# Kernel tuning notes

Hardware: AMD Instinct MI355X
Metric: run time of the kernel (lower is better)

The kernel has to match this reference:

```python
import jax, jax.numpy as jnp
import numpy as np

DN = ('NCDHW', 'OIDHW', 'NCDHW')


def conv3d(x, w, b, stride=2, pad=1):
    # w: [Cout, Cin, k, k, k] (PyTorch Conv3d layout == OIDHW)
    y = jax.lax.conv_general_dilated(x, w, (stride,) * 3, [(pad, pad)] * 3,
                                     dimension_numbers=DN)
    return y + b[None, :, None, None, None]


def convT3d(x, w, b, stride=2, pad=1):
    # w: [Cin, Cout, k, k, k] (PyTorch ConvTranspose3d layout).
    # ConvTranspose(k,s,p) == conv(lhs_dilated by s, flipped kernel, pad = k-1-p)
    k = w.shape[2]
    wf = jnp.transpose(jnp.flip(w, (2, 3, 4)), (1, 0, 2, 3, 4))  # -> OIDHW
    p = k - 1 - pad
    y = jax.lax.conv_general_dilated(x, wf, (1, 1, 1), [(p, p)] * 3,
                                     lhs_dilation=(stride,) * 3,
                                     dimension_numbers=DN)
    return y + b[None, :, None, None, None]


def setup_inputs() -> dict:
    key = jax.random.key(0)
    ks = jax.random.split(key, 14)
    s = 0.05
    inp = {
        'x': jax.random.normal(ks[0], (4, 1, 128, 128, 128), jnp.float32),
        # encoder conv weights (OIDHW) + biases
        'w1': jax.random.normal(ks[1], (16, 1, 4, 4, 4), jnp.float32) * s,
        'b1': jnp.zeros((16,), jnp.float32),
        'w2': jax.random.normal(ks[2], (32, 16, 4, 4, 4), jnp.float32) * s,
        'b2': jnp.zeros((32,), jnp.float32),
        'w3': jax.random.normal(ks[3], (64, 32, 4, 4, 4), jnp.float32) * s,
        'b3': jnp.zeros((64,), jnp.float32),
        # VQ codebook [num_embeddings=512, latent_dim=64]
        'codebook': jax.random.normal(ks[4], (512, 64), jnp.float32),
        # decoder conv-transpose weights (PyTorch layout: [Cin, Cout, k,k,k]) + biases
        'dw1': jax.random.normal(ks[5], (64, 32, 4, 4, 4), jnp.float32) * s,
        'db1': jnp.zeros((32,), jnp.float32),
        'dw2': jax.random.normal(ks[6], (32, 16, 4, 4, 4), jnp.float32) * s,
        'db2': jnp.zeros((16,), jnp.float32),
        'dw3': jax.random.normal(ks[7], (16, 1, 4, 4, 4), jnp.float32) * s,
        'db3': jnp.zeros((1,), jnp.float32),
    }
    return inp


def reference(x, w1, b1, w2, b2, w3, b3, codebook, dw1, db1, dw2, db2, dw3, db3):
    # ---- encoder ----
    h = jax.nn.relu(conv3d(x, w1, b1))
    h = jax.nn.relu(conv3d(h, w2, b2))
    z_e = conv3d(h, w3, b3)                      # [B, C=64, D, H, W]
    B, C, D, H, W = z_e.shape

    # ---- vector quantization (cdist + argmin + gather) ----
    zf = jnp.transpose(z_e.reshape(B, C, -1), (0, 2, 1))   # [B, N, C]
    # squared euclidean distances (argmin identical to cdist argmin)
    d2 = (jnp.sum(zf * zf, axis=-1, keepdims=True)
          + jnp.sum(codebook * codebook, axis=-1)[None, None, :]
          - 2.0 * jnp.einsum('bnc,kc->bnk', zf, codebook))  # [B, N, K]
    encoding_indices = jnp.argmin(d2, axis=-1)              # [B, N]
    q = codebook[encoding_indices]                          # [B, N, C]
    quantized = jnp.transpose(q, (0, 2, 1)).reshape(B, C, D, H, W)
    # straight-through estimator
    quantized = z_e + jax.lax.stop_gradient(quantized - z_e)

    # ---- decoder ----
    h = jax.nn.relu(convT3d(quantized, dw1, db1))
    h = jax.nn.relu(convT3d(h, dw2, db2))
    x_hat = jax.nn.sigmoid(convT3d(h, dw3, db3))
    return (x_hat, quantized, z_e)
```

## Files before the change

### kernel.cpp

```cpp
#include <hip/hip_runtime.h>
#include <math.h>


__device__ __forceinline__ float4 ld4(const float* p) {
  float4 q; __builtin_memcpy(&q, p, 16); return q;
}
struct F3 { float x, y, z; };
__device__ __forceinline__ F3 ld3(const float* p) {
  F3 q; __builtin_memcpy(&q, p, 12); return q;
}

#define WAVES_HINT __attribute__((amdgpu_waves_per_eu(2, 4)))

template<int CIN, int COUT>
__global__ __launch_bounds__(256) void k_repackT(const float* __restrict__ w,
                                                 float* __restrict__ dst) {
  const int idx = blockIdx.x * 256 + threadIdx.x;
  if (idx >= CIN * 8 * COUT * 8) return;
  const int a  = idx & 7;
  const int co = (idx >> 3) % COUT;
  const int p  = ((idx >> 3) / COUT) & 7;
  const int ci2 = idx / (8 * COUT * 8);
  const int az = a >> 2, ay = (a >> 1) & 1, ax = a & 1;
  const int pz = p >> 2, py = (p >> 1) & 1, px = p & 1;
  const int kz = 3 - pz - 2 * az, ky = 3 - py - 2 * ay, kx = 3 - px - 2 * ax;
  dst[(((size_t)(ci2 * 8 + p) * COUT + co) * 16) + az * 8 + (ay * 2 + ax)] =
      w[((size_t)ci2 * COUT + co) * 64 + (kz * 16 + ky * 4 + kx)];
}

template<int S, int D, int NCH>
__global__ __launch_bounds__(256) void k_zhalo(float* __restrict__ buf) {
  const int vol = S * S * S;
  const long long idx = (long long)blockIdx.x * 256 + threadIdx.x;
  if (idx >= (long long)NCH * vol) return;
  const int r = (int)(idx % vol);
  const int z = r / (S * S), y = (r / S) % S, x = r % S;
  if (z < 1 || z > D || y < 1 || y > D || x < 1 || x > D) buf[idx] = 0.0f;
}

template<int CIN, int COUT, int DIN, int DOUT, int OCG, int TZ, bool RELU,
         bool INP, int SIN, bool OUTP, int SOUT, int NG>
__global__ __launch_bounds__(256) WAVES_HINT
void k_conv(const float* __restrict__ xin, const float* __restrict__ wg,
            const float* __restrict__ bias, float* __restrict__ out) {
  constexpr int NBX = DOUT / 8, NBY = DOUT / 8, NBZ = DOUT / (4 * TZ);
  constexpr size_t VIN  = INP  ? (size_t)SIN * SIN * SIN : (size_t)DIN * DIN * DIN;
  constexpr size_t VOUT = OUTP ? (size_t)SOUT * SOUT * SOUT : (size_t)DOUT * DOUT * DOUT;
  const int tid = threadIdx.x;
  const int tx = tid & 7, ty = (tid >> 3) & 7, tz = tid >> 6;
  int bb = blockIdx.x;
  const int g  = bb % NG;  bb /= NG;
  const int gx = bb % NBX; bb /= NBX;
  const int gy = bb % NBY; bb /= NBY;
  const int gz = bb % NBZ; bb /= NBZ;
  const int b = bb;
  const int oc0 = g * OCG;
  const int ow = gx * 8 + tx, oh = gy * 8 + ty, od0 = gz * (4 * TZ) + tz;

  float acc[TZ][OCG];
#pragma unroll
  for (int j = 0; j < TZ; ++j)
#pragma unroll
    for (int c = 0; c < OCG; ++c) acc[j][c] = 0.0f;

#pragma unroll 1
  for (int ci = 0; ci < CIN; ++ci) {
    const float* xb = xin + (size_t)(b * CIN + ci) * VIN;
#pragma unroll 1
    for (int t16 = 0; t16 < 16; ++t16) {
      float4 q[TZ];
      if (INP) {
        const int zp = od0 * 2 + (t16 >> 2);
        const int yp = oh * 2 + (t16 & 3);
        const float* r0 = xb + ((size_t)zp * SIN + yp) * SIN + ow * 2;
#pragma unroll
        for (int j = 0; j < TZ; ++j) q[j] = ld4(r0 + (size_t)j * 8 * SIN * SIN);
      } else {
        const int y  = oh * 2 - 1 + (t16 & 3);
        const int x0 = ow * 2 - 1;
        const bool vy = (unsigned)y < (unsigned)DIN;
#pragma unroll
        for (int j = 0; j < TZ; ++j) {
          const int z = od0 * 2 - 1 + (t16 >> 2) + j * 8;
          const bool vz = vy && ((unsigned)z < (unsigned)DIN);
          const float* xr = xb + ((size_t)z * DIN + y) * DIN + x0;
          q[j].x = (vz && (unsigned)(x0 + 0) < (unsigned)DIN) ? xr[0] : 0.0f;
          q[j].y = (vz && (unsigned)(x0 + 1) < (unsigned)DIN) ? xr[1] : 0.0f;
          q[j].z = (vz && (unsigned)(x0 + 2) < (unsigned)DIN) ? xr[2] : 0.0f;
          q[j].w = (vz && (unsigned)(x0 + 3) < (unsigned)DIN) ? xr[3] : 0.0f;
        }
      }
#pragma unroll
      for (int c = 0; c < OCG; ++c) {
        const float4 w4 = ld4(wg + ((size_t)(oc0 + c) * CIN + ci) * 64 + t16 * 4);
#pragma unroll
        for (int j = 0; j < TZ; ++j) {
          acc[j][c] = fmaf(q[j].x, w4.x, acc[j][c]);
          acc[j][c] = fmaf(q[j].y, w4.y, acc[j][c]);
          acc[j][c] = fmaf(q[j].z, w4.z, acc[j][c]);
          acc[j][c] = fmaf(q[j].w, w4.w, acc[j][c]);
        }
      }
    }
  }

#pragma unroll
  for (int c = 0; c < OCG; ++c) {
    const float bv = bias[oc0 + c];
#pragma unroll
    for (int j = 0; j < TZ; ++j) {
      float v = acc[j][c] + bv;
      if (RELU) v = fmaxf(v, 0.0f);
      const int od = od0 + j * 4;
      if (OUTP)
        out[(size_t)(b * COUT + oc0 + c) * VOUT
            + ((size_t)(od + 1) * SOUT + (oh + 1)) * SOUT + (ow + 1)] = v;
      else
        out[(size_t)(b * COUT + oc0 + c) * VOUT
            + ((size_t)od * DOUT + oh) * DOUT + ow] = v;
    }
  }
}

template<int CIN, int COUT, int DIN, int OCG, int TZ, int EPI, int SIN,
         bool OUTP, int SOUT, int NG>
__global__ __launch_bounds__(256) WAVES_HINT
void k_convt(const float* __restrict__ xin, const float* __restrict__ wp,
             const float* __restrict__ bias, float* __restrict__ out) {
  constexpr int DOUT = 2 * DIN, NBX = DIN / 8, NBY = DIN / 8,
                NBZ = DIN / (4 * TZ);
  constexpr size_t VIN  = (size_t)SIN * SIN * SIN;
  constexpr size_t VOUT = OUTP ? (size_t)SOUT * SOUT * SOUT
                               : (size_t)DOUT * DOUT * DOUT;
  const int tid = threadIdx.x;
  const int tx = tid & 7, ty = (tid >> 3) & 7, tz = tid >> 6;
  int bb = blockIdx.x;
  const int g  = bb % NG;  bb /= NG;
  const int gx = bb % NBX; bb /= NBX;
  const int gy = bb % NBY; bb /= NBY;
  const int gz = bb % NBZ; bb /= NBZ;
  const int b = bb;
  const int oc0 = g * OCG;
  const int mx = gx * 8 + tx, my = gy * 8 + ty;
  const int mz0 = gz * (4 * TZ) + tz * TZ;

  float acc[TZ][8][OCG];
#pragma unroll
  for (int j = 0; j < TZ; ++j)
#pragma unroll
    for (int p = 0; p < 8; ++p)
#pragma unroll
      for (int c = 0; c < OCG; ++c) acc[j][p][c] = 0.0f;

#pragma unroll 1
  for (int ci = 0; ci < CIN; ++ci) {
    const float* xb = xin + (size_t)(b * CIN + ci) * VIN
                          + ((size_t)mz0 * SIN + my) * SIN + mx;
    float xn[TZ + 2][3][3];
#pragma unroll
    for (int dz = 0; dz < TZ + 2; ++dz)
#pragma unroll
      for (int dy = 0; dy < 3; ++dy) {
        const F3 t = ld3(xb + ((size_t)dz * SIN + dy) * SIN);
        xn[dz][dy][0] = t.x; xn[dz][dy][1] = t.y; xn[dz][dy][2] = t.z;
      }
    __builtin_amdgcn_sched_barrier(0);

    const float* wci = wp + (size_t)ci * 8 * COUT * 16;
#pragma unroll
    for (int p = 0; p < 8; ++p) {
      const int pz = p >> 2, py = (p >> 1) & 1, px = p & 1;
#pragma unroll
      for (int c = 0; c < OCG; ++c) {
        const float* wb = wci + ((size_t)p * COUT + (oc0 + c)) * 16;
        const float4 wA = ld4(wb);
        const float4 wB = ld4(wb + 8);
#pragma unroll
        for (int j = 0; j < TZ; ++j)
          acc[j][p][c] = fmaf(xn[j + pz][py    ][px    ], wA.x, acc[j][p][c]);
#pragma unroll
        for (int j = 0; j < TZ; ++j)
          acc[j][p][c] = fmaf(xn[j + pz][py    ][px + 1], wA.y, acc[j][p][c]);
#pragma unroll
        for (int j = 0; j < TZ; ++j)
          acc[j][p][c] = fmaf(xn[j + pz][py + 1][px    ], wA.z, acc[j][p][c]);
#pragma unroll
        for (int j = 0; j < TZ; ++j)
          acc[j][p][c] = fmaf(xn[j + pz][py + 1][px + 1], wA.w, acc[j][p][c]);
#pragma unroll
        for (int j = 0; j < TZ; ++j)
          acc[j][p][c] = fmaf(xn[j + pz + 1][py    ][px    ], wB.x, acc[j][p][c]);
#pragma unroll
        for (int j = 0; j < TZ; ++j)
          acc[j][p][c] = fmaf(xn[j + pz + 1][py    ][px + 1], wB.y, acc[j][p][c]);
#pragma unroll
        for (int j = 0; j < TZ; ++j)
          acc[j][p][c] = fmaf(xn[j + pz + 1][py + 1][px    ], wB.z, acc[j][p][c]);
#pragma unroll
        for (int j = 0; j < TZ; ++j)
          acc[j][p][c] = fmaf(xn[j + pz + 1][py + 1][px + 1], wB.w, acc[j][p][c]);
      }
    }
  }

#pragma unroll
  for (int c = 0; c < OCG; ++c) {
    const float bv = bias[oc0 + c];
#pragma unroll
    for (int j = 0; j < TZ; ++j) {
      const int mz = mz0 + j;
#pragma unroll
      for (int p = 0; p < 8; ++p) {
        const int pz = p >> 2, py = (p >> 1) & 1, px = p & 1;
        float v = acc[j][p][c] + bv;
        if (EPI == 1) v = fmaxf(v, 0.0f);
        if (EPI == 2) v = 1.0f / (1.0f + expf(-v));
        if (OUTP)
          out[(size_t)(b * COUT + oc0 + c) * VOUT
              + ((size_t)(2 * mz + pz + 1) * SOUT + (2 * my + py + 1)) * SOUT
              + (2 * mx + px + 1)] = v;
        else
          out[(size_t)(b * COUT + oc0 + c) * VOUT
              + ((size_t)(2 * mz + pz) * DOUT + (2 * my + py)) * DOUT
              + (2 * mx + px)] = v;
      }
    }
  }
}

__global__ __launch_bounds__(256) void k_vq(const float* __restrict__ ze,
                                            const float* __restrict__ cb,
                                            float* __restrict__ quant,
                                            float* __restrict__ quantp) {
  __shared__ float ct[64 * 65];
  __shared__ float zs[4][64];
  __shared__ int   bis[4];
  const int tid  = threadIdx.x;
  const int lane = tid & 63;
  const int wv   = tid >> 6;
  const int p0 = blockIdx.x * 4;
  const int b  = p0 >> 12;
  const int n0 = p0 & 4095;

  {
    const int c = tid >> 2, j = tid & 3;
    zs[j][c] = ze[((size_t)(b * 64 + c) << 12) + n0 + j];
  }

  float best = 3.4e38f;
  int bi = 0;
#pragma unroll 1
  for (int ch = 0; ch < 8; ++ch) {
    __syncthreads();
    for (int i = tid; i < 4096; i += 256) {
      const int r = i >> 6, c = i & 63;
      ct[r * 65 + c] = cb[((ch * 64 + r) << 6) + c];
    }
    __syncthreads();
    float d = 0.0f;
#pragma unroll 8
    for (int c = 0; c < 64; ++c) {
      const float t = zs[wv][c] - ct[lane * 65 + c];
      d = fmaf(t, t, d);
    }
    const int k = ch * 64 + lane;
    if (d < best) { best = d; bi = k; }
  }
#pragma unroll
  for (int off = 32; off > 0; off >>= 1) {
    const float ob = __shfl_down(best, off);
    const int   oi = __shfl_down(bi, off);
    if (ob < best || (ob == best && oi < bi)) { best = ob; bi = oi; }
  }
  if (lane == 0) bis[wv] = bi;
  __syncthreads();
  {
    const int c = tid >> 2, j = tid & 3;
    const float val = cb[(bis[j] << 6) + c];
    const int n = n0 + j;
    quant[((size_t)(b * 64 + c) << 12) + n] = val;
    const int zz = n >> 8, yy = (n >> 4) & 15, xx = n & 15;
    quantp[(size_t)(b * 64 + c) * 8000
           + ((size_t)(zz + 1) * 20 + (yy + 1)) * 20 + (xx + 1)] = val;
  }
}

extern "C" void kernel_launch(void* const* d_in, const int* in_sizes, int n_in,
                              void* d_out, int out_size, void* d_ws, size_t ws_size,
                              hipStream_t stream) {
  const float* x   = (const float*)d_in[0];
  const float* w1  = (const float*)d_in[1];
  const float* b1  = (const float*)d_in[2];
  const float* w2  = (const float*)d_in[3];
  const float* b2  = (const float*)d_in[4];
  const float* w3  = (const float*)d_in[5];
  const float* b3  = (const float*)d_in[6];
  const float* cb  = (const float*)d_in[7];
  const float* dw1 = (const float*)d_in[8];
  const float* db1 = (const float*)d_in[9];
  const float* dw2 = (const float*)d_in[10];
  const float* db2 = (const float*)d_in[11];
  const float* dw3 = (const float*)d_in[12];
  const float* db3 = (const float*)d_in[13];

  float* outf  = (float*)d_out;
  float* xhat  = outf;
  float* quant = outf + 8388608;
  float* ze    = outf + 9437184;

  float* regA = (float*)d_ws;
  float* regB = regA + (size_t)64 * 68 * 68 * 68;
  float* regC = regB + (size_t)128 * 36 * 36 * 36;
  float* t1p = regC + (size_t)256 * 20 * 20 * 20;
  float* t2p = t1p + 262144;
  float* t3p = t2p + 65536;

  k_repackT<64, 32><<<512, 256, 0, stream>>>(dw1, t1p);
  k_repackT<32, 16><<<128, 256, 0, stream>>>(dw2, t2p);
  k_repackT<16, 1><<<4, 256, 0, stream>>>(dw3, t3p);
  k_zhalo<68, 64, 64><<<78608, 256, 0, stream>>>(regA);
  k_zhalo<36, 32, 128><<<23328, 256, 0, stream>>>(regB);
  k_zhalo<20, 16, 256><<<8000, 256, 0, stream>>>(regC);

  k_conv<1, 16, 128, 64, 16, 2, true, false, 0, true, 68, 1>
      <<<2048, 256, 0, stream>>>(x, w1, b1, regA);
  k_conv<16, 32, 64, 32, 16, 1, true, true, 68, true, 36, 2>
      <<<1024, 256, 0, stream>>>(regA, w2, b2, regB);
  k_conv<32, 64, 32, 16, 4, 1, false, true, 36, false, 16, 16>
      <<<1024, 256, 0, stream>>>(regB, w3, b3, ze);
  k_vq<<<4096, 256, 0, stream>>>(ze, cb, quant, regC);
  k_convt<64, 32, 16, 2, 1, 1, 20, true, 36, 16>
      <<<1024, 256, 0, stream>>>(regC, t1p, db1, regB);
  k_convt<32, 16, 32, 2, 4, 1, 36, true, 68, 8>
      <<<1024, 256, 0, stream>>>(regB, t2p, db2, regA);
  k_convt<16, 1, 64, 1, 4, 2, 68, false, 0, 1>
      <<<1024, 256, 0, stream>>>(regA, t3p, db3, xhat);
}
```

Measured before the change: 1.053 ms.

## Software-pipeline input loads in multi-channel encoder conv with register double buffering

Splits the encoder conv kernel into a single-channel path and a multi-channel path. The multi-channel path prefetches the next kz-slab of input rows (4 rows × TZ) into a double-buffered register array while FMAs run on the current slab, with a sched_barrier to keep the loads issued early. The goal is to hide global load latency behind arithmetic. In exchange it roughly doubles the input registers per thread, which may lower occupancy or cause spills, and it requires padded input.

```diff
diff --git a/kernel.cpp b/kernel.cpp
--- a/kernel.cpp
+++ b/kernel.cpp
@@ -63,9 +63,8 @@
 #pragma unroll
     for (int c = 0; c < OCG; ++c) acc[j][c] = 0.0f;
 
-#pragma unroll 1
-  for (int ci = 0; ci < CIN; ++ci) {
-    const float* xb = xin + (size_t)(b * CIN + ci) * VIN;
+  if constexpr (CIN == 1) {
+    const float* xb = xin + (size_t)b * VIN;
 #pragma unroll 1
     for (int t16 = 0; t16 < 16; ++t16) {
       float4 q[TZ];
@@ -92,13 +91,56 @@
       }
 #pragma unroll
       for (int c = 0; c < OCG; ++c) {
-        const float4 w4 = ld4(wg + ((size_t)(oc0 + c) * CIN + ci) * 64 + t16 * 4);
+        const float4 w4 = ld4(wg + (size_t)(oc0 + c) * 64 + t16 * 4);
 #pragma unroll
         for (int j = 0; j < TZ; ++j) {
           acc[j][c] = fmaf(q[j].x, w4.x, acc[j][c]);
           acc[j][c] = fmaf(q[j].y, w4.y, acc[j][c]);
           acc[j][c] = fmaf(q[j].z, w4.z, acc[j][c]);
           acc[j][c] = fmaf(q[j].w, w4.w, acc[j][c]);
+        }
+      }
+    }
+  } else {
+    static_assert(!(CIN > 1) || INP, "pipelined path requires padded input");
+    const float* xb0 = xin + (size_t)b * CIN * VIN
+                     + (((size_t)(od0 * 2) * SIN + oh * 2) * SIN + ow * 2);
+
+    auto loadg = [&](float4 (&qb)[4][TZ], int ci, int gg) {
+      const float* base = xb0 + (size_t)ci * VIN + (size_t)gg * SIN * SIN;
+#pragma unroll
+      for (int t = 0; t < 4; ++t)
+#pragma unroll
+        for (int j = 0; j < TZ; ++j)
+          qb[t][j] = ld4(base + (size_t)t * SIN + (size_t)j * 8 * SIN * SIN);
+    };
+
+    float4 q[2][4][TZ];
+    loadg(q[0], 0, 0);
+
+#pragma unroll 1
+    for (int ci = 0; ci < CIN; ++ci) {
+#pragma unroll
+      for (int kg = 0; kg < 4; ++kg) {
+        const int nci = (kg == 3) ? ci + 1 : ci;
+        const int ngg = (kg == 3) ? 0 : kg + 1;
+        if (nci < CIN) loadg(q[(kg + 1) & 1], nci, ngg);
+        __builtin_amdgcn_sched_barrier(0);
+#pragma unroll
+        for (int t = 0; t < 4; ++t) {
+          const int t16 = kg * 4 + t;
+#pragma unroll
+          for (int c = 0; c < OCG; ++c) {
+            const float4 w4 =
+                ld4(wg + ((size_t)(oc0 + c) * CIN + ci) * 64 + t16 * 4);
+#pragma unroll
+            for (int j = 0; j < TZ; ++j) {
+              acc[j][c] = fmaf(q[kg & 1][t][j].x, w4.x, acc[j][c]);
+              acc[j][c] = fmaf(q[kg & 1][t][j].y, w4.y, acc[j][c]);
+              acc[j][c] = fmaf(q[kg & 1][t][j].z, w4.z, acc[j][c]);
+              acc[j][c] = fmaf(q[kg & 1][t][j].w, w4.w, acc[j][c]);
+            }
+          }
         }
       }
     }
```

Result: slower. 1.324 ms (+25.7%).
